# Performance work log

Measured on AMD Instinct MI355X. Metric: run time of the kernel, lower is better.

Reference implementation:

```python
import jax, jax.numpy as jnp
import numpy as np

H = 768       # hidden_dim
NH = 12       # num_heads
HD = H // NH  # head_dim = 64


def setup_inputs() -> dict:
    key = jax.random.key(0)
    ks = jax.random.split(key, 5)
    scale = 1.0 / np.sqrt(H)
    x = jax.random.normal(ks[0], (16, 1024, H), dtype=jnp.float32)
    W_qkv = jax.random.normal(ks[1], (H, 3 * H), dtype=jnp.float32) * scale
    b_qkv = jnp.zeros((3 * H,), dtype=jnp.float32)
    W_proj = jax.random.normal(ks[2], (H, H), dtype=jnp.float32) * scale
    b_proj = jnp.zeros((H,), dtype=jnp.float32)
    return {"x": x, "W_qkv": W_qkv, "b_qkv": b_qkv, "W_proj": W_proj, "b_proj": b_proj}


def reference(x, W_qkv, b_qkv, W_proj, b_proj):
    bsz, seq_len, hidden = x.shape
    qkv = x @ W_qkv + b_qkv                              # [B,S,3H]
    q, k, v = jnp.split(qkv, 3, axis=-1)
    def heads(t):
        return t.reshape(bsz, seq_len, NH, HD).transpose(0, 2, 1, 3)  # [B,NH,S,HD]
    q, k, v = heads(q), heads(k), heads(v)
    scores = jnp.einsum('bhqd,bhkd->bhqk', q, k) / jnp.sqrt(jnp.float32(HD))
    causal = jnp.tril(jnp.ones((seq_len, seq_len), dtype=bool))
    scores = jnp.where(causal, scores, jnp.finfo(scores.dtype).min)
    attn = jax.nn.softmax(scores, axis=-1)
    out = jnp.einsum('bhqk,bhkd->bhqd', attn, v)         # [B,NH,S,HD]
    out = out.transpose(0, 2, 1, 3).reshape(bsz, seq_len, hidden)
    return out @ W_proj + b_proj
```

## Files before the change

kernel.cpp:

```cpp
#include <hip/hip_runtime.h>

#define H 768
#define NH 12
#define HD 64
#define BSZ 16
#define SEQ 1024
#define MTOK (BSZ * SEQ)
#define N3H (3 * H)

typedef __attribute__((ext_vector_type(8))) short bf16x8;
typedef __attribute__((ext_vector_type(4))) float f32x4;
typedef __attribute__((ext_vector_type(16))) float f32x16;
typedef __attribute__((ext_vector_type(8))) unsigned short us8;
typedef __attribute__((ext_vector_type(4))) unsigned short us4;

__device__ __forceinline__ unsigned short f2bf(float f) {
    union { float f; unsigned u; } v; v.f = f;
    unsigned r = v.u + 0x7fffu + ((v.u >> 16) & 1u);
    return (unsigned short)(r >> 16);
}

typedef __attribute__((address_space(1))) const unsigned int gu32_t;
typedef __attribute__((address_space(3))) unsigned int lu32_t;
__device__ __forceinline__ void glds16(const void* g, void* l) {
    __builtin_amdgcn_global_load_lds((gu32_t*)g, (lu32_t*)l, 16, 0, 0);
}

__global__ __launch_bounds__(256) void prep(
    const float* __restrict__ x,
    const float* __restrict__ Wqkv, const float* __restrict__ Wproj,
    unsigned short* __restrict__ xbf,
    unsigned short* __restrict__ wqkvT, unsigned short* __restrict__ wprojT)
{
    __shared__ float tile[64][65];
    int bx = blockIdx.x, t = threadIdx.x;

    if (bx < 6144) {
        int i = bx * 2048 + t * 8;
        float4 a = *(const float4*)(x + i);
        float4 b = *(const float4*)(x + i + 4);
        us8 o;
        o[0]=f2bf(a.x); o[1]=f2bf(a.y); o[2]=f2bf(a.z); o[3]=f2bf(a.w);
        o[4]=f2bf(b.x); o[5]=f2bf(b.y); o[6]=f2bf(b.z); o[7]=f2bf(b.w);
        *(us8*)(xbf + i) = o;
        return;
    }

    const float* in; unsigned short* out; int Kd, Nd, n0, k0;
    if (bx < 6576) {
        int lb = bx - 6144;
        in = Wqkv; out = wqkvT; Kd = H; Nd = N3H;
        n0 = (lb % 36) * 64; k0 = (lb / 36) * 64;
    } else {
        int lb = bx - 6576;
        in = Wproj; out = wprojT; Kd = H; Nd = H;
        n0 = (lb % 12) * 64; k0 = (lb / 12) * 64;
    }
    #pragma unroll
    for (int r = 0; r < 4; ++r) {
        int kl = r * 16 + (t >> 4);
        float4 v = *(const float4*)(&in[(size_t)(k0 + kl) * Nd + n0 + (t & 15) * 4]);
        tile[kl][(t & 15) * 4 + 0] = v.x; tile[kl][(t & 15) * 4 + 1] = v.y;
        tile[kl][(t & 15) * 4 + 2] = v.z; tile[kl][(t & 15) * 4 + 3] = v.w;
    }
    __syncthreads();
    int nl = t >> 2, kc = (t & 3) * 16;
    us8 o0, o1;
    #pragma unroll
    for (int kk = 0; kk < 8; ++kk) o0[kk] = f2bf(tile[kc + kk][nl]);
    #pragma unroll
    for (int kk = 0; kk < 8; ++kk) o1[kk] = f2bf(tile[kc + 8 + kk][nl]);
    size_t ob = (size_t)(n0 + nl) * Kd + k0 + kc;
    *(us8*)(&out[ob]) = o0;
    *(us8*)(&out[ob + 8]) = o1;
}

__global__ __launch_bounds__(256) void gemm_bf16(
    const unsigned short* __restrict__ A, const unsigned short* __restrict__ BT,
    const float* __restrict__ bias, void* __restrict__ Cout,
    int M, int N, int K, int write_f32, int qscale_end)
{
    __shared__ char lds[49152];
    char* As = lds;
    char* Bs = lds + 32768;
    const char* Ac = (const char*)A;
    const char* Bc = (const char*)BT;
    int t = threadIdx.x;
    int l = t & 63, w = t >> 6;
    int l31 = l & 31, b5 = l >> 5;

    int chunk = (int)gridDim.x >> 3;
    int lin = (blockIdx.x & 7) * chunk + (blockIdx.x >> 3);
    int nbx = N >> 7;
    int bx = lin % nbx, by = lin / nbx;
    int rowBase = by * 256, colBase = bx * 128;

    f32x16 acc[2][4];
    #pragma unroll
    for (int mi = 0; mi < 2; ++mi)
        #pragma unroll
        for (int ni = 0; ni < 4; ++ni)
            #pragma unroll
            for (int r = 0; r < 16; ++r) acc[mi][ni][r] = 0.f;

    for (int k0 = 0; k0 < K; k0 += 64) {
        #pragma unroll
        for (int i = 0; i < 8; ++i) {
            int c = t + i * 256;
            int row = c >> 3;
            int src = ((c & 7) * 16) ^ ((row & 7) << 4);
            glds16(Ac + ((size_t)(rowBase + row) * K + k0) * 2 + src, As + c * 16);
        }
        #pragma unroll
        for (int i = 0; i < 4; ++i) {
            int c = t + i * 256;
            int row = c >> 3;
            int src = ((c & 7) * 16) ^ ((row & 7) << 4);
            glds16(Bc + ((size_t)(colBase + row) * K + k0) * 2 + src, Bs + c * 16);
        }
        asm volatile("s_waitcnt vmcnt(0)" ::: "memory");
        __builtin_amdgcn_s_barrier();

        #pragma unroll
        for (int ks = 0; ks < 4; ++ks) {
            bf16x8 af[2], bfr[4];
            #pragma unroll
            for (int mi = 0; mi < 2; ++mi) {
                int row = w * 64 + mi * 32 + l31;
                af[mi] = *(const bf16x8*)(As + row * 128 + ((ks * 32 + b5 * 16) ^ ((row & 7) << 4)));
            }
            #pragma unroll
            for (int ni = 0; ni < 4; ++ni) {
                int row = ni * 32 + l31;
                bfr[ni] = *(const bf16x8*)(Bs + row * 128 + ((ks * 32 + b5 * 16) ^ ((row & 7) << 4)));
            }
            #pragma unroll
            for (int mi = 0; mi < 2; ++mi)
                #pragma unroll
                for (int ni = 0; ni < 4; ++ni)
                    acc[mi][ni] = __builtin_amdgcn_mfma_f32_32x32x16_bf16(
                        af[mi], bfr[ni], acc[mi][ni], 0, 0, 0);
        }
        __builtin_amdgcn_s_barrier();
    }

    #pragma unroll
    for (int ni = 0; ni < 4; ++ni) {
        int col = colBase + ni * 32 + l31;
        float bb = bias ? bias[col] : 0.f;
        float mul = (col < qscale_end) ? 0.125f : 1.0f;
        #pragma unroll
        for (int mi = 0; mi < 2; ++mi) {
            #pragma unroll
            for (int reg = 0; reg < 16; ++reg) {
                int row = rowBase + w * 64 + mi * 32 + (reg & 3) + 8 * (reg >> 2) + 4 * b5;
                float v = (acc[mi][ni][reg] + bb) * mul;
                if (write_f32) ((float*)Cout)[(size_t)row * N + col] = v;
                else ((unsigned short*)Cout)[(size_t)row * N + col] = f2bf(v);
            }
        }
    }
}

__global__ __launch_bounds__(256) void vtrans(
    const unsigned short* __restrict__ qkvb, unsigned short* __restrict__ vt)
{
    __shared__ char tile[64 * 128];
    int t = threadIdx.x;
    int st = blockIdx.x, h = blockIdx.y, b = blockIdx.z;
    int s0 = st * 64;
    {
        int s = t >> 2, dc = (t & 3) * 16;
        size_t g = (size_t)(b * SEQ + s0 + s) * N3H + 2 * H + h * HD + dc;
        us8 v0 = *(const us8*)(&qkvb[g]);
        us8 v1 = *(const us8*)(&qkvb[g + 8]);
        *(us8*)(tile + s * 128 + ((dc * 2) ^ ((s & 7) << 4))) = v0;
        *(us8*)(tile + s * 128 + ((dc * 2 + 16) ^ ((s & 7) << 4))) = v1;
    }
    __syncthreads();
    int d = t >> 2, sc = (t & 3) * 16;
    us8 o0, o1;
    #pragma unroll
    for (int kk = 0; kk < 8; ++kk) {
        int s = sc + kk;
        o0[kk] = *(const unsigned short*)(tile + s * 128 + ((d * 2) ^ ((s & 7) << 4)));
    }
    #pragma unroll
    for (int kk = 0; kk < 8; ++kk) {
        int s = sc + 8 + kk;
        o1[kk] = *(const unsigned short*)(tile + s * 128 + ((d * 2) ^ ((s & 7) << 4)));
    }
    size_t ob = ((size_t)((b * NH + h) * 64 + d)) * SEQ + s0 + sc;
    *(us8*)(&vt[ob]) = o0;
    *(us8*)(&vt[ob + 8]) = o1;
}

__global__ __launch_bounds__(256, 4) void attn_mfma(
    const unsigned short* __restrict__ qkvb,
    const unsigned short* __restrict__ vt,
    unsigned short* __restrict__ aout)
{
    __shared__ char lds[32768];
    char* Kbuf = lds;
    char* Vbuf = lds + 16384;
    int t = threadIdx.x;
    int l = t & 63, w = t >> 6;
    int l31 = l & 31, b5 = l >> 5;

    int lin = ((blockIdx.x & 7) * 192) + (blockIdx.x >> 3);
    int qb = 7 - (lin & 7);
    int bh = lin >> 3;
    int h = bh % NH, b = bh / NH;

    int wq = qb * 128 + w * 32;
    int sw31 = (l31 & 7) << 4;
    int nt = 2 * qb + 2;
    int bhh = b * NH + h;
    const char* qkvc = (const char*)qkvb;
    const char* vtc  = (const char*)vt;

    bf16x8 qB[4];
    {
        const unsigned short* qrow =
            qkvb + (size_t)(b * SEQ + wq + l31) * N3H + h * HD + b5 * 8;
        #pragma unroll
        for (int m = 0; m < 4; ++m) qB[m] = *(const bf16x8*)(qrow + m * 16);
    }

    auto STAGE = [&](int kt, int bi) {
        #pragma unroll
        for (int i = 0; i < 2; ++i) {
            int c = t + i * 256;
            int row = c >> 3;
            int src = ((c & 7) * 16) ^ ((row & 7) << 4);
            glds16(qkvc + ((size_t)(b * SEQ + kt * 64 + row) * N3H + H + h * HD) * 2 + src,
                   Kbuf + bi * 8192 + c * 16);
        }
        #pragma unroll
        for (int i = 0; i < 2; ++i) {
            int c = t + i * 256;
            int row = c >> 3;
            int src = ((c & 7) * 16) ^ ((row & 7) << 4);
            glds16(vtc + (((size_t)(bhh * 64 + row)) * SEQ + kt * 64) * 2 + src,
                   Vbuf + bi * 8192 + c * 16);
        }
    };

    STAGE(0, 0);
    __syncthreads();

    f32x16 o0, o1;
    #pragma unroll
    for (int r = 0; r < 16; ++r) { o0[r] = 0.f; o1[r] = 0.f; }
    float mrun = -1e30f, lrun = 0.f;

    for (int kt = 0; kt < nt; ++kt) {
        int bi = kt & 1;
        if (kt + 1 < nt) {
            STAGE(kt + 1, bi ^ 1);
            asm volatile("s_waitcnt vmcnt(4)" ::: "memory");
        } else {
            asm volatile("s_waitcnt vmcnt(0)" ::: "memory");
        }
        __builtin_amdgcn_s_barrier();

        int ktbase = kt * 64;
        if (ktbase <= wq + 31) {
            const char* Kb = Kbuf + bi * 8192;
            const char* Vb = Vbuf + bi * 8192;
            bool two = (ktbase + 32 <= wq + 31);

            f32x16 s0, s1;
            __builtin_amdgcn_s_setprio(1);
            {
                f32x16 a;
                #pragma unroll
                for (int r = 0; r < 16; ++r) a[r] = 0.f;
                #pragma unroll
                for (int m = 0; m < 4; ++m) {
                    bf16x8 kf = *(const bf16x8*)(Kb + l31 * 128 + ((m * 32 + b5 * 16) ^ sw31));
                    a = __builtin_amdgcn_mfma_f32_32x32x16_bf16(kf, qB[m], a, 0, 0, 0);
                }
                s0 = a;
            }
            if (two) {
                f32x16 a;
                #pragma unroll
                for (int r = 0; r < 16; ++r) a[r] = 0.f;
                #pragma unroll
                for (int m = 0; m < 4; ++m) {
                    bf16x8 kf = *(const bf16x8*)(Kb + (32 + l31) * 128 + ((m * 32 + b5 * 16) ^ sw31));
                    a = __builtin_amdgcn_mfma_f32_32x32x16_bf16(kf, qB[m], a, 0, 0, 0);
                }
                s1 = a;
            }
            __builtin_amdgcn_s_setprio(0);

            int q = wq + l31;
            if (ktbase + 31 > wq) {
                #pragma unroll
                for (int r = 0; r < 16; ++r) {
                    int key = ktbase + (r & 3) + 8 * (r >> 2) + 4 * b5;
                    if (key > q) s0[r] = -3e38f;
                }
            }
            if (two && (ktbase + 63 > wq)) {
                #pragma unroll
                for (int r = 0; r < 16; ++r) {
                    int key = ktbase + 32 + (r & 3) + 8 * (r >> 2) + 4 * b5;
                    if (key > q) s1[r] = -3e38f;
                }
            }

            float m01 = fmaxf(s0[0], s0[1]), m23 = fmaxf(s0[2], s0[3]);
            float m45 = fmaxf(s0[4], s0[5]), m67 = fmaxf(s0[6], s0[7]);
            float m89 = fmaxf(s0[8], s0[9]), mab = fmaxf(s0[10], s0[11]);
            float mcd = fmaxf(s0[12], s0[13]), mef = fmaxf(s0[14], s0[15]);
            float mx = fmaxf(fmaxf(fmaxf(m01, m23), fmaxf(m45, m67)),
                             fmaxf(fmaxf(m89, mab), fmaxf(mcd, mef)));
            if (two) {
                float n01 = fmaxf(s1[0], s1[1]), n23 = fmaxf(s1[2], s1[3]);
                float n45 = fmaxf(s1[4], s1[5]), n67 = fmaxf(s1[6], s1[7]);
                float n89 = fmaxf(s1[8], s1[9]), nab = fmaxf(s1[10], s1[11]);
                float ncd = fmaxf(s1[12], s1[13]), nef = fmaxf(s1[14], s1[15]);
                mx = fmaxf(mx, fmaxf(fmaxf(fmaxf(n01, n23), fmaxf(n45, n67)),
                                     fmaxf(fmaxf(n89, nab), fmaxf(ncd, nef))));
            }
            mx = fmaxf(mx, __shfl_xor(mx, 32, 64));
            if (!__all(mx - mrun <= 8.f)) {
                float mnew = fmaxf(mrun, mx);
                float sc = __expf(mrun - mnew);
                mrun = mnew;
                lrun *= sc;
                #pragma unroll
                for (int r = 0; r < 16; ++r) { o0[r] *= sc; o1[r] *= sc; }
            }
            float rs = 0.f;
            #pragma unroll
            for (int r = 0; r < 16; ++r) {
                float p = __expf(s0[r] - mrun);
                s0[r] = p;
                rs += p;
            }
            if (two) {
                #pragma unroll
                for (int r = 0; r < 16; ++r) {
                    float p = __expf(s1[r] - mrun);
                    s1[r] = p;
                    rs += p;
                }
            }
            rs += __shfl_xor(rs, 32, 64);
            lrun += rs;

            bf16x8 pB[4];
            #pragma unroll
            for (int wd = 0; wd < 4; ++wd) {
                if (wd >= 2 && !two) break;
                const f32x16& sv = (wd < 2) ? s0 : s1;
                int hf = (wd & 1) * 8;
                unsigned pk0 = (unsigned)f2bf(sv[hf + 0]) | ((unsigned)f2bf(sv[hf + 1]) << 16);
                unsigned pk1 = (unsigned)f2bf(sv[hf + 2]) | ((unsigned)f2bf(sv[hf + 3]) << 16);
                unsigned pk2 = (unsigned)f2bf(sv[hf + 4]) | ((unsigned)f2bf(sv[hf + 5]) << 16);
                unsigned pk3 = (unsigned)f2bf(sv[hf + 6]) | ((unsigned)f2bf(sv[hf + 7]) << 16);
                unsigned snd0 = b5 ? pk0 : pk2;
                unsigned snd1 = b5 ? pk1 : pk3;
                unsigned r0 = (unsigned)__shfl_xor((int)snd0, 32, 64);
                unsigned r1 = (unsigned)__shfl_xor((int)snd1, 32, 64);
                union { unsigned u[4]; bf16x8 v; } cvt;
                cvt.u[0] = b5 ? r0 : pk0;
                cvt.u[1] = b5 ? r1 : pk1;
                cvt.u[2] = b5 ? pk2 : r0;
                cvt.u[3] = b5 ? pk3 : r1;
                pB[wd] = cvt.v;
            }

            __builtin_amdgcn_s_setprio(1);
            #pragma unroll
            for (int wd = 0; wd < 4; ++wd) {
                if (wd >= 2 && !two) break;
                bf16x8 v0 = *(const bf16x8*)(Vb + l31 * 128 + ((wd * 32 + b5 * 16) ^ sw31));
                o0 = __builtin_amdgcn_mfma_f32_32x32x16_bf16(v0, pB[wd], o0, 0, 0, 0);
                bf16x8 v1 = *(const bf16x8*)(Vb + (32 + l31) * 128 + ((wd * 32 + b5 * 16) ^ sw31));
                o1 = __builtin_amdgcn_mfma_f32_32x32x16_bf16(v1, pB[wd], o1, 0, 0, 0);
            }
            __builtin_amdgcn_s_setprio(0);
        }
        __builtin_amdgcn_s_barrier();
    }

    float inv = 1.f / lrun;
    size_t tok = (size_t)(b * SEQ + wq + l31);
    #pragma unroll
    for (int g = 0; g < 4; ++g) {
        us4 w0, w1;
        #pragma unroll
        for (int j = 0; j < 4; ++j) {
            w0[j] = f2bf(o0[g * 4 + j] * inv);
            w1[j] = f2bf(o1[g * 4 + j] * inv);
        }
        int d0 = g * 8 + b5 * 4;
        *(us4*)(&aout[tok * H + h * HD + d0]) = w0;
        *(us4*)(&aout[tok * H + h * HD + 32 + d0]) = w1;
    }
}

extern "C" void kernel_launch(void* const* d_in, const int* in_sizes, int n_in,
                              void* d_out, int out_size, void* d_ws, size_t ws_size,
                              hipStream_t stream) {
    const float* x      = (const float*)d_in[0];
    const float* W_qkv  = (const float*)d_in[1];
    const float* b_qkv  = (const float*)d_in[2];
    const float* W_proj = (const float*)d_in[3];
    const float* b_proj = (const float*)d_in[4];
    float* outp = (float*)d_out;

    char* ws = (char*)d_ws;
    unsigned short* xbf    = (unsigned short*)ws;  ws += (size_t)MTOK * H * 2;
    unsigned short* wqkvT  = (unsigned short*)ws;  ws += (size_t)N3H * H * 2;
    unsigned short* wprojT = (unsigned short*)ws;  ws += (size_t)H * H * 2;
    unsigned short* qkvb   = (unsigned short*)ws;  ws += (size_t)MTOK * N3H * 2;
    unsigned short* vtb    = (unsigned short*)ws;  ws += (size_t)BSZ * NH * 64 * SEQ * 2;
    unsigned short* aob    = (unsigned short*)ws;

    prep<<<6720, 256, 0, stream>>>(x, W_qkv, W_proj, xbf, wqkvT, wprojT);

    gemm_bf16<<<(MTOK / 256) * (N3H / 128), 256, 0, stream>>>(
        xbf, wqkvT, b_qkv, qkvb, MTOK, N3H, H, 0, H);

    vtrans<<<dim3(SEQ / 64, NH, BSZ), 256, 0, stream>>>(qkvb, vtb);

    attn_mfma<<<(SEQ / 128) * NH * BSZ, 256, 0, stream>>>(qkvb, vtb, aob);

    gemm_bf16<<<(MTOK / 256) * (H / 128), 256, 0, stream>>>(
        aob, wprojT, b_proj, (void*)outp, MTOK, H, H, 1, 0);
}
```

Baseline: 379.5 us.

## Fuse V transpose into QKV GEMM epilogue and retile GEMM to 128x128 with 16x16 MFMA

The QKV GEMM epilogue now writes V columns directly in the transposed per-head layout, which removes the separate vtrans kernel and its extra pass over V. The GEMM also moves from a 256x128 tile using 32x32x16 MFMA to a 128x128 tile using 16x16x32 MFMA on a 2x2 wave grid. The smaller tile cuts LDS use and doubles the block count, at the cost of more operand loads per FLOP. The transposed V stores are 8-byte strided writes, which may coalesce poorly.

```diff
diff --git a/kernel.cpp b/kernel.cpp
--- a/kernel.cpp
+++ b/kernel.cpp
@@ -78,121 +78,109 @@
 __global__ __launch_bounds__(256) void gemm_bf16(
     const unsigned short* __restrict__ A, const unsigned short* __restrict__ BT,
     const float* __restrict__ bias, void* __restrict__ Cout,
+    unsigned short* __restrict__ vt,
     int M, int N, int K, int write_f32, int qscale_end)
 {
-    __shared__ char lds[49152];
+    __shared__ char lds[32768];
     char* As = lds;
-    char* Bs = lds + 32768;
+    char* Bs = lds + 16384;
     const char* Ac = (const char*)A;
     const char* Bc = (const char*)BT;
     int t = threadIdx.x;
     int l = t & 63, w = t >> 6;
-    int l31 = l & 31, b5 = l >> 5;
+    int l16 = l & 15, l4 = l >> 4;
+    int wm = w >> 1, wn = w & 1;
 
     int chunk = (int)gridDim.x >> 3;
     int lin = (blockIdx.x & 7) * chunk + (blockIdx.x >> 3);
     int nbx = N >> 7;
     int bx = lin % nbx, by = lin / nbx;
-    int rowBase = by * 256, colBase = bx * 128;
-
-    f32x16 acc[2][4];
-    #pragma unroll
-    for (int mi = 0; mi < 2; ++mi)
-        #pragma unroll
-        for (int ni = 0; ni < 4; ++ni)
-            #pragma unroll
-            for (int r = 0; r < 16; ++r) acc[mi][ni][r] = 0.f;
+    int rowBase = by * 128, colBase = bx * 128;
+
+    f32x4 acc[4][4];
+    #pragma unroll
+    for (int i = 0; i < 4; ++i)
+        #pragma unroll
+        for (int j = 0; j < 4; ++j) acc[i][j] = (f32x4){0, 0, 0, 0};
 
     for (int k0 = 0; k0 < K; k0 += 64) {
         #pragma unroll
-        for (int i = 0; i < 8; ++i) {
+        for (int i = 0; i < 4; ++i) {
             int c = t + i * 256;
             int row = c >> 3;
             int src = ((c & 7) * 16) ^ ((row & 7) << 4);
             glds16(Ac + ((size_t)(rowBase + row) * K + k0) * 2 + src, As + c * 16);
-        }
-        #pragma unroll
-        for (int i = 0; i < 4; ++i) {
-            int c = t + i * 256;
-            int row = c >> 3;
-            int src = ((c & 7) * 16) ^ ((row & 7) << 4);
             glds16(Bc + ((size_t)(colBase + row) * K + k0) * 2 + src, Bs + c * 16);
         }
         asm volatile("s_waitcnt vmcnt(0)" ::: "memory");
         __builtin_amdgcn_s_barrier();
 
         #pragma unroll
-        for (int ks = 0; ks < 4; ++ks) {
-            bf16x8 af[2], bfr[4];
-            #pragma unroll
-            for (int mi = 0; mi < 2; ++mi) {
-                int row = w * 64 + mi * 32 + l31;
-                af[mi] = *(const bf16x8*)(As + row * 128 + ((ks * 32 + b5 * 16) ^ ((row & 7) << 4)));
+        for (int kh = 0; kh < 2; ++kh) {
+            bf16x8 af[4], bfr[4];
+            #pragma unroll
+            for (int mi = 0; mi < 4; ++mi) {
+                int row = wm * 64 + mi * 16 + l16;
+                af[mi] = *(const bf16x8*)(As + row * 128 + ((l4 * 16 + kh * 64) ^ ((row & 7) << 4)));
             }
             #pragma unroll
             for (int ni = 0; ni < 4; ++ni) {
-                int row = ni * 32 + l31;
-                bfr[ni] = *(const bf16x8*)(Bs + row * 128 + ((ks * 32 + b5 * 16) ^ ((row & 7) << 4)));
-            }
-            #pragma unroll
-            for (int mi = 0; mi < 2; ++mi)
+                int row = wn * 64 + ni * 16 + l16;
+                bfr[ni] = *(const bf16x8*)(Bs + row * 128 + ((l4 * 16 + kh * 64) ^ ((row & 7) << 4)));
+            }
+            #pragma unroll
+            for (int mi = 0; mi < 4; ++mi)
                 #pragma unroll
                 for (int ni = 0; ni < 4; ++ni)
-                    acc[mi][ni] = __builtin_amdgcn_mfma_f32_32x32x16_bf16(
+                    acc[mi][ni] = __builtin_amdgcn_mfma_f32_16x16x32_bf16(
                         af[mi], bfr[ni], acc[mi][ni], 0, 0, 0);
         }
         __builtin_amdgcn_s_barrier();
     }
 
-    #pragma unroll
-    for (int ni = 0; ni < 4; ++ni) {
-        int col = colBase + ni * 32 + l31;
-        float bb = bias ? bias[col] : 0.f;
-        float mul = (col < qscale_end) ? 0.125f : 1.0f;
-        #pragma unroll
-        for (int mi = 0; mi < 2; ++mi) {
-            #pragma unroll
-            for (int reg = 0; reg < 16; ++reg) {
-                int row = rowBase + w * 64 + mi * 32 + (reg & 3) + 8 * (reg >> 2) + 4 * b5;
-                float v = (acc[mi][ni][reg] + bb) * mul;
-                if (write_f32) ((float*)Cout)[(size_t)row * N + col] = v;
-                else ((unsigned short*)Cout)[(size_t)row * N + col] = f2bf(v);
-            }
-        }
-    }
-}
-
-__global__ __launch_bounds__(256) void vtrans(
-    const unsigned short* __restrict__ qkvb, unsigned short* __restrict__ vt)
-{
-    __shared__ char tile[64 * 128];
-    int t = threadIdx.x;
-    int st = blockIdx.x, h = blockIdx.y, b = blockIdx.z;
-    int s0 = st * 64;
-    {
-        int s = t >> 2, dc = (t & 3) * 16;
-        size_t g = (size_t)(b * SEQ + s0 + s) * N3H + 2 * H + h * HD + dc;
-        us8 v0 = *(const us8*)(&qkvb[g]);
-        us8 v1 = *(const us8*)(&qkvb[g + 8]);
-        *(us8*)(tile + s * 128 + ((dc * 2) ^ ((s & 7) << 4))) = v0;
-        *(us8*)(tile + s * 128 + ((dc * 2 + 16) ^ ((s & 7) << 4))) = v1;
-    }
-    __syncthreads();
-    int d = t >> 2, sc = (t & 3) * 16;
-    us8 o0, o1;
-    #pragma unroll
-    for (int kk = 0; kk < 8; ++kk) {
-        int s = sc + kk;
-        o0[kk] = *(const unsigned short*)(tile + s * 128 + ((d * 2) ^ ((s & 7) << 4)));
-    }
-    #pragma unroll
-    for (int kk = 0; kk < 8; ++kk) {
-        int s = sc + 8 + kk;
-        o1[kk] = *(const unsigned short*)(tile + s * 128 + ((d * 2) ^ ((s & 7) << 4)));
-    }
-    size_t ob = ((size_t)((b * NH + h) * 64 + d)) * SEQ + s0 + sc;
-    *(us8*)(&vt[ob]) = o0;
-    *(us8*)(&vt[ob + 8]) = o1;
+    if (write_f32) {
+        #pragma unroll
+        for (int ni = 0; ni < 4; ++ni) {
+            int col = colBase + wn * 64 + ni * 16 + l16;
+            float bb = bias ? bias[col] : 0.f;
+            #pragma unroll
+            for (int mi = 0; mi < 4; ++mi) {
+                #pragma unroll
+                for (int j = 0; j < 4; ++j) {
+                    int row = rowBase + wm * 64 + mi * 16 + l4 * 4 + j;
+                    ((float*)Cout)[(size_t)row * N + col] = acc[mi][ni][j] + bb;
+                }
+            }
+        }
+    } else {
+        #pragma unroll
+        for (int ni = 0; ni < 4; ++ni) {
+            int col = colBase + wn * 64 + ni * 16 + l16;
+            float bb = bias ? bias[col] : 0.f;
+            float mul = (col < qscale_end) ? 0.125f : 1.0f;
+            bool isV = vt && (col >= 2 * H);
+            #pragma unroll
+            for (int mi = 0; mi < 4; ++mi) {
+                int row0 = rowBase + wm * 64 + mi * 16 + l4 * 4;
+                if (isV) {
+                    us4 ov;
+                    #pragma unroll
+                    for (int j = 0; j < 4; ++j) ov[j] = f2bf(acc[mi][ni][j] + bb);
+                    int dfull = col - 2 * H;
+                    int hh = dfull >> 6, dd = dfull & 63;
+                    int bq = row0 >> 10, s = row0 & 1023;
+                    *(us4*)(&vt[((size_t)((bq * NH + hh) * 64 + dd)) * SEQ + s]) = ov;
+                } else {
+                    #pragma unroll
+                    for (int j = 0; j < 4; ++j) {
+                        int row = row0 + j;
+                        ((unsigned short*)Cout)[(size_t)row * N + col] =
+                            f2bf((acc[mi][ni][j] + bb) * mul);
+                    }
+                }
+            }
+        }
+    }
 }
 
 __global__ __launch_bounds__(256, 4) void attn_mfma(
@@ -425,13 +413,11 @@
 
     prep<<<6720, 256, 0, stream>>>(x, W_qkv, W_proj, xbf, wqkvT, wprojT);
 
-    gemm_bf16<<<(MTOK / 256) * (N3H / 128), 256, 0, stream>>>(
-        xbf, wqkvT, b_qkv, qkvb, MTOK, N3H, H, 0, H);
-
-    vtrans<<<dim3(SEQ / 64, NH, BSZ), 256, 0, stream>>>(qkvb, vtb);
+    gemm_bf16<<<(N3H / 128) * (MTOK / 128), 256, 0, stream>>>(
+        xbf, wqkvT, b_qkv, qkvb, vtb, MTOK, N3H, H, 0, H);
 
     attn_mfma<<<(SEQ / 128) * NH * BSZ, 256, 0, stream>>>(qkvb, vtb, aob);
 
-    gemm_bf16<<<(MTOK / 256) * (H / 128), 256, 0, stream>>>(
-        aob, wprojT, b_proj, (void*)outp, MTOK, H, H, 1, 0);
-}
+    gemm_bf16<<<(H / 128) * (MTOK / 128), 256, 0, stream>>>(
+        aob, wprojT, b_proj, (void*)outp, nullptr, MTOK, H, H, 1, 0);
+}
```

New measurement: 318.9 us. 16.0% less time.
